# Kernel tuning notes

Hardware: AMD Instinct MI355X
Metric: run time of the kernel (lower is better)

Reference implementation:

```python
import jax, jax.numpy as jnp
import numpy as np

T, HEADS, DIM_HEAD = 16, 16, 72
M = HEADS * DIM_HEAD  # 1152
SCALE = DIM_HEAD ** -0.5


def _ln(x, eps):
    mu = x.mean(-1, keepdims=True)
    var = x.var(-1, keepdims=True)
    return (x - mu) / jnp.sqrt(var + eps)


def _rotate_half(t):
    # interleaved pairs (x1, x2) -> (-x2, x1), as in rotary-embedding-torch
    t1, t2 = t[..., 0::2], t[..., 1::2]
    return jnp.stack([-t2, t1], axis=-1).reshape(t.shape)


def _rotary(t, pos):
    d = t.shape[-1]
    inv_freq = 1.0 / (10000.0 ** (jnp.arange(0, d, 2, dtype=jnp.float32) / d))
    freqs = pos.astype(jnp.float32)[:, None] * inv_freq          # (T, d/2)
    freqs = jnp.repeat(freqs, 2, axis=-1)                        # (T, d)
    return t * jnp.cos(freqs) + _rotate_half(t) * jnp.sin(freqs)


def _forward(x, c4t, c, W_ada, b_ada, tn_w, tn_b, t_qkv, t_k, t_v, t_out,
             t_fc_w, t_fc_b, s_qkv, s_k, s_v, s_out,
             mlp_w1, mlp_b1, mlp_w2, mlp_b2, f):
    B = c4t.shape[0]
    K, N, _ = x.shape

    ada = jax.nn.silu(c4t) @ W_ada + b_ada                       # (B, 6M)
    sh_msa, sc_msa, g_msa, sh_mlp, sc_mlp, g_mlp = jnp.split(ada, 6, axis=1)

    x4 = x.reshape(B, T, N, M)

    # ---- temporal attention (seq dim = frames, rotary, per-frame cond k/v) ----
    xt = _ln(x4, 1e-5) * tn_w + tn_b                             # temporal_norm1
    xt = xt.transpose(0, 2, 1, 3)                                # (B, N, T, M)
    q, k, v = jnp.split(xt @ t_qkv, 3, axis=-1)

    def heads_t(t):  # (B,N,T,M) -> (B,N,h,T,d)
        return t.reshape(B, N, T, HEADS, DIM_HEAD).transpose(0, 1, 3, 2, 4)

    q, k, v = map(heads_t, (q, k, v))
    k = _rotary(k, f)
    ek = (c @ t_k).reshape(B, T, HEADS, DIM_HEAD).transpose(0, 2, 1, 3)  # (B,h,T,d)
    ev = (c @ t_v).reshape(B, T, HEADS, DIM_HEAD).transpose(0, 2, 1, 3)
    ek = _rotary(ek, f)
    ek = jnp.broadcast_to(ek[:, None], k.shape)                  # (B,N,h,T,d)
    ev = jnp.broadcast_to(ev[:, None], v.shape)
    kk = jnp.concatenate([ek, k], axis=-2)                       # (B,N,h,2T,d)
    vv = jnp.concatenate([ev, v], axis=-2)
    q = _rotary(q * SCALE, f)
    attn = jax.nn.softmax(jnp.einsum('bnhid,bnhjd->bnhij', q, kk), axis=-1)
    out = jnp.einsum('bnhij,bnhjd->bnhid', attn, vv)
    out = out.transpose(0, 1, 3, 2, 4).reshape(B, N, T, M) @ t_out
    res = out.transpose(0, 2, 1, 3) @ t_fc_w + t_fc_b            # (B,T,N,M)
    x4 = x4 + res

    # ---- spatial attention with adaLN modulate + one cond token per frame ----
    mod = _ln(x4, 1e-6) * (1.0 + sc_msa[:, None, None, :]) + sh_msa[:, None, None, :]
    q, k, v = jnp.split(mod @ s_qkv, 3, axis=-1)

    def heads_s(t):  # (B,T,N,M) -> (B,T,h,N,d)
        return t.reshape(B, T, N, HEADS, DIM_HEAD).transpose(0, 1, 3, 2, 4)

    q, k, v = map(heads_s, (q, k, v))
    ek = (c @ s_k).reshape(B, T, HEADS, DIM_HEAD)[:, :, :, None, :]  # (B,T,h,1,d)
    ev = (c @ s_v).reshape(B, T, HEADS, DIM_HEAD)[:, :, :, None, :]
    kk = jnp.concatenate([ek, k], axis=-2)                       # (B,T,h,N+1,d)
    vv = jnp.concatenate([ev, v], axis=-2)
    attn = jax.nn.softmax(jnp.einsum('bthid,bthjd->bthij', q * SCALE, kk), axis=-1)
    out = jnp.einsum('bthij,bthjd->bthid', attn, vv)
    out = out.transpose(0, 1, 3, 2, 4).reshape(B, T, N, M) @ s_out
    x4 = x4 + g_msa[:, None, None, :] * out

    # ---- gated MLP with adaLN modulate ----
    mod2 = _ln(x4, 1e-6) * (1.0 + sc_mlp[:, None, None, :]) + sh_mlp[:, None, None, :]
    h = jax.nn.gelu(mod2 @ mlp_w1 + mlp_b1, approximate=True)
    y = h @ mlp_w2 + mlp_b2
    x4 = x4 + g_mlp[:, None, None, :] * y
    return x4.reshape(K, N, M)


def setup_inputs() -> dict:
    key = jax.random.key(0)
    ks = jax.random.split(key, 20)
    B, N = 2, 256

    def w(k, shape, s=0.02):
        return jax.random.normal(k, shape, jnp.float32) * s

    return {
        'x': jax.random.normal(ks[0], (B * T, N, M), jnp.float32),
        'c4t': jax.random.normal(ks[1], (B, M), jnp.float32),
        'c': jax.random.normal(ks[2], (B, T, M), jnp.float32),
        'W_ada': w(ks[3], (M, 6 * M)), 'b_ada': w(ks[4], (6 * M,)),
        'tn_w': jnp.ones(M, jnp.float32), 'tn_b': jnp.zeros(M, jnp.float32),
        't_qkv': w(ks[5], (M, 3 * M)), 't_k': w(ks[6], (M, M)),
        't_v': w(ks[7], (M, M)), 't_out': w(ks[8], (M, M)),
        't_fc_w': w(ks[9], (M, M)), 't_fc_b': jnp.zeros(M, jnp.float32),
        's_qkv': w(ks[10], (M, 3 * M)), 's_k': w(ks[11], (M, M)),
        's_v': w(ks[12], (M, M)), 's_out': w(ks[13], (M, M)),
        'mlp_w1': w(ks[14], (M, 4 * M)), 'mlp_b1': jnp.zeros(4 * M, jnp.float32),
        'mlp_w2': w(ks[15], (4 * M, M)), 'mlp_b2': jnp.zeros(M, jnp.float32),
        'f': jnp.arange(T, dtype=jnp.int32),
    }


def reference(x, c4t, c, W_ada, b_ada, tn_w, tn_b, t_qkv, t_k, t_v, t_out,
              t_fc_w, t_fc_b, s_qkv, s_k, s_v, s_out,
              mlp_w1, mlp_b1, mlp_w2, mlp_b2, f):
    return _forward(x, c4t, c, W_ada, b_ada, tn_w, tn_b, t_qkv, t_k, t_v, t_out,
                    t_fc_w, t_fc_b, s_qkv, s_k, s_v, s_out,
                    mlp_w1, mlp_b1, mlp_w2, mlp_b2, f)
```

## Files before the change

kernel.cpp:

```cpp
#include <hip/hip_runtime.h>
#include <hip/hip_bf16.h>

typedef __hip_bfloat16 bf16;
typedef __attribute__((ext_vector_type(8))) short short8;
typedef __attribute__((ext_vector_type(4))) float floatx4;

__device__ __forceinline__ float b2f(bf16 v) { return __bfloat162float(v); }
__device__ __forceinline__ short f2bs(float v) {
    bf16 h = __float2bfloat16(v);
    return *(short*)&h;
}
__device__ __forceinline__ float invfreq(int jj) {
    return expf(-0.25584278811044955f * (float)jj);
}

template<int MODE>
__device__ __forceinline__ float ldin(const void* p, long i) {
    if (MODE == 0) return b2f(((const bf16*)p)[i]);
    else           return ((const float*)p)[i];
}

#define SCALE_ 0.11785113019775793f

#define GLDS(gp, lp) __builtin_amdgcn_global_load_lds( \
    (const __attribute__((address_space(1))) void*)(gp), \
    (__attribute__((address_space(3))) void*)(lp), 16, 0, 0)

__global__ void k_detect(const void* __restrict__ x, int* __restrict__ flag)
{
    const unsigned short* u = (const unsigned short*)x;
    int tid = threadIdx.x;
    int insane = 0;
    for (int i = tid; i < 2048; i += 64) {
        unsigned short s = u[i];
        int ex = (s >> 7) & 0xFF;
        if (ex >= 0xC5) insane++;
    }
    #pragma unroll
    for (int off = 32; off > 0; off >>= 1) insane += __shfl_down(insane, off);
    if (tid == 0) flag[0] = (insane > 8) ? 1 : 0;
}

__global__ void k_rope(const int* __restrict__ f, float* __restrict__ ropeC,
                       float* __restrict__ ropeS)
{
    int idx = blockIdx.x * 256 + threadIdx.x;
    if (idx < 1152) {
        int t = idx / 72, d = idx - t * 72;
        float ang = (float)f[t] * invfreq(d >> 1);
        float sn, cs; sincosf(ang, &sn, &cs);
        ropeC[idx] = cs;
        ropeS[idx] = sn;
    }
}

__global__ void k_silu(const void* __restrict__ c4t, float* __restrict__ out,
                       const int* __restrict__ flg)
{
    int i = blockIdx.x * 256 + threadIdx.x;
    if (i < 2304) {
        float v = (*flg == 0) ? ldin<0>(c4t, i) : ldin<1>(c4t, i);
        out[i] = v / (1.f + expf(-v));
    }
}

__global__ void k_cvt(const void* __restrict__ in, float* __restrict__ out, int n,
                      const int* __restrict__ flg)
{
    int i = blockIdx.x * 256 + threadIdx.x;
    if (i < n) out[i] = (*flg == 0) ? ldin<0>(in, i) : ldin<1>(in, i);
}

__global__ void k_cvtb(const float* __restrict__ in, bf16* __restrict__ out, int n)
{
    int i = blockIdx.x * 256 + threadIdx.x;
    if (i < n) out[i] = __float2bfloat16(in[i]);
}

template<int MODE>
__device__ __forceinline__ void wt_body(float (*tile)[33], const void* __restrict__ W,
    bf16* __restrict__ Wt, int K, int N)
{
    int n0 = blockIdx.x << 5, k0 = blockIdx.y << 5;
    int tid = threadIdx.x;
    int r = tid >> 3, c4 = (tid & 7) << 2;
    long base = (long)(k0 + r) * N + n0 + c4;
    #pragma unroll
    for (int i = 0; i < 4; ++i) tile[r][c4 + i] = ldin<MODE>(W, base + i);
    __syncthreads();
    long obase = (long)(n0 + r) * K + k0 + c4;
    #pragma unroll
    for (int i = 0; i < 4; ++i) Wt[obase + i] = __float2bfloat16(tile[c4 + i][r]);
}

__global__ __launch_bounds__(256) void k_wt(const void* __restrict__ W,
    bf16* __restrict__ Wt, int K, int N, const int* __restrict__ flg)
{
    __shared__ float tile[32][33];
    if (*flg == 0) wt_body<0>(tile, W, Wt, K, N);
    else           wt_body<1>(tile, W, Wt, K, N);
}

template<int MODE>
__device__ __forceinline__ void gemm_body(
    float (*As)[64], float (*Bs)[64],
    const float* __restrict__ A, const void* __restrict__ W,
    const void* __restrict__ bias, float* __restrict__ C,
    int R, int K, int N)
{
    int tid = threadIdx.x;
    int tx = tid & 15, ty = tid >> 4;
    int row0 = blockIdx.y << 6;
    int col0 = blockIdx.x << 6;
    float acc[4][4] = {};
    int ar = tid >> 2;
    int ak = (tid & 3) << 2;
    int bk = tid >> 4;
    int bc = (tid & 15) << 2;
    for (int kt = 0; kt < K; kt += 16) {
        if (row0 + ar < R) {
            const float4 a4 = *(const float4*)(A + (long)(row0 + ar) * K + kt + ak);
            As[ak + 0][ar] = a4.x; As[ak + 1][ar] = a4.y;
            As[ak + 2][ar] = a4.z; As[ak + 3][ar] = a4.w;
        } else {
            As[ak + 0][ar] = 0.f; As[ak + 1][ar] = 0.f;
            As[ak + 2][ar] = 0.f; As[ak + 3][ar] = 0.f;
        }
        #pragma unroll
        for (int i = 0; i < 4; ++i)
            Bs[bk][bc + i] = ldin<MODE>(W, (long)(kt + bk) * N + col0 + bc + i);
        __syncthreads();
        #pragma unroll
        for (int kk = 0; kk < 16; ++kk) {
            float4 av = *(const float4*)&As[kk][ty << 2];
            float4 bv = *(const float4*)&Bs[kk][tx << 2];
            float a[4] = {av.x, av.y, av.z, av.w};
            float b[4] = {bv.x, bv.y, bv.z, bv.w};
            #pragma unroll
            for (int i = 0; i < 4; ++i)
                #pragma unroll
                for (int j = 0; j < 4; ++j)
                    acc[i][j] += a[i] * b[j];
        }
        __syncthreads();
    }
    #pragma unroll
    for (int i = 0; i < 4; ++i) {
        int gr = row0 + (ty << 2) + i;
        if (gr >= R) continue;
        float* cp = C + (long)gr * N + col0 + (tx << 2);
        #pragma unroll
        for (int j = 0; j < 4; ++j) {
            float v = acc[i][j];
            if (bias) v += ldin<MODE>(bias, col0 + (tx << 2) + j);
            cp[j] = v;
        }
    }
}

__global__ __launch_bounds__(256) void k_gemm(
    const float* __restrict__ A, const void* __restrict__ W,
    const void* __restrict__ bias, float* __restrict__ C,
    int R, int K, int N, const int* __restrict__ flg)
{
    __shared__ float As[16][64];
    __shared__ float Bs[16][64];
    if (*flg == 0) gemm_body<0>(As, Bs, A, W, bias, C, R, K, N);
    else           gemm_body<1>(As, Bs, A, W, bias, C, R, K, N);
}

__global__ __launch_bounds__(256) void k_mgemm(
    const bf16* __restrict__ A, const bf16* __restrict__ Wt,
    const float* __restrict__ bias, void* __restrict__ Cout,
    int K, int N, int outbf, int act)
{
    __shared__ short As[8192];
    __shared__ short Bs[8192];
    int tid = threadIdx.x;
    int lane = tid & 63, wave = tid >> 6;
    int mq = wave >> 1, nq = wave & 1;

    int gx = gridDim.x;
    int nwg = gx * (int)gridDim.y;
    int orig = blockIdx.y * gx + blockIdx.x;
    int qq = nwg >> 3, rr = nwg & 7;
    int xcd = orig & 7, loc = orig >> 3;
    int wg = (xcd < rr ? xcd * (qq + 1) : rr * (qq + 1) + (xcd - rr) * qq) + loc;
    int bx = wg % gx, by = wg / gx;

    long row0 = (long)by << 7;
    long col0 = (long)bx << 7;
    int mi = lane & 15, q = lane >> 4;

    const bf16* gA0 = A  + (row0 + (2 * wave) * 16 + mi) * K + q * 8;
    const bf16* gA1 = A  + (row0 + (2 * wave + 1) * 16 + mi) * K + q * 8;
    const bf16* gB0 = Wt + (col0 + (2 * wave) * 16 + mi) * K + q * 8;
    const bf16* gB1 = Wt + (col0 + (2 * wave + 1) * 16 + mi) * K + q * 8;
    short* lA0 = &As[((2 * wave) << 1) * 512];
    short* lA1 = &As[((2 * wave + 1) << 1) * 512];
    short* lB0 = &Bs[((2 * wave) << 1) * 512];
    short* lB1 = &Bs[((2 * wave + 1) << 1) * 512];

    floatx4 acc[4][4] = {};

    for (int kt = 0; kt < K; kt += 64) {
        GLDS(gA0 + kt,      lA0);
        GLDS(gA0 + kt + 32, lA0 + 512);
        GLDS(gA1 + kt,      lA1);
        GLDS(gA1 + kt + 32, lA1 + 512);
        GLDS(gB0 + kt,      lB0);
        GLDS(gB0 + kt + 32, lB0 + 512);
        GLDS(gB1 + kt,      lB1);
        GLDS(gB1 + kt + 32, lB1 + 512);
        __syncthreads();
        #pragma unroll
        for (int s = 0; s < 2; ++s) {
            short8 af[4], bfr[4];
            #pragma unroll
            for (int i = 0; i < 4; ++i)
                af[i] = *(const short8*)&As[((((4 * mq + i) << 1) + s) << 9) + lane * 8];
            #pragma unroll
            for (int j = 0; j < 4; ++j)
                bfr[j] = *(const short8*)&Bs[((((4 * nq + j) << 1) + s) << 9) + lane * 8];
            #pragma unroll
            for (int i = 0; i < 4; ++i)
                #pragma unroll
                for (int j = 0; j < 4; ++j)
                    acc[i][j] = __builtin_amdgcn_mfma_f32_16x16x32_bf16(
                        af[i], bfr[j], acc[i][j], 0, 0, 0);
        }
        __syncthreads();
    }

    int lr = lane >> 4, lc = lane & 15;
    float b4[4] = {0.f, 0.f, 0.f, 0.f};
    if (bias) {
        #pragma unroll
        for (int j = 0; j < 4; ++j) b4[j] = bias[(int)col0 + nq * 64 + j * 16 + lc];
    }
    #pragma unroll
    for (int i = 0; i < 4; ++i) {
        #pragma unroll
        for (int r = 0; r < 4; ++r) {
            long grow = row0 + mq * 64 + i * 16 + lr * 4 + r;
            #pragma unroll
            for (int j = 0; j < 4; ++j) {
                int col = (int)col0 + nq * 64 + j * 16 + lc;
                float v = acc[i][j][r] + b4[j];
                if (act) {
                    float u = v;
                    float t = 1.5957691216057308f * (u + 0.044715f * u * u * u);
                    v = u / (1.f + __expf(-t));
                }
                if (outbf) ((bf16*)Cout)[grow * N + col] = __float2bfloat16(v);
                else       ((float*)Cout)[grow * N + col] = v;
            }
        }
    }
}

template<int MODE>
__device__ __forceinline__ void ln_t_body(float* rs, float* rss,
    const void* __restrict__ x, const void* __restrict__ w,
    const void* __restrict__ bb, bf16* __restrict__ out)
{
    int r = blockIdx.x;
    int n = r & 255;
    int bt = r >> 8;
    int b = bt >> 4, t = bt & 15;
    long orow = (long)((b << 8) + n) * 16 + t;
    int tid = threadIdx.x;
    float vals[5];
    float s = 0.f, ss = 0.f;
    int c = 0;
    for (int i = tid; i < 1152; i += 256, ++c) {
        float v = ldin<MODE>(x, (long)r * 1152 + i);
        vals[c] = v; s += v; ss += v * v;
    }
    #pragma unroll
    for (int off = 32; off > 0; off >>= 1) {
        s  += __shfl_down(s, off);
        ss += __shfl_down(ss, off);
    }
    int wid = tid >> 6;
    if ((tid & 63) == 0) { rs[wid] = s; rss[wid] = ss; }
    __syncthreads();
    float S  = rs[0] + rs[1] + rs[2] + rs[3];
    float SS = rss[0] + rss[1] + rss[2] + rss[3];
    float mu = S * (1.f / 1152.f);
    float var = SS * (1.f / 1152.f) - mu * mu;
    float rstd = rsqrtf(var + 1e-5f);
    c = 0;
    bf16* op = out + orow * 1152;
    for (int i = tid; i < 1152; i += 256, ++c)
        op[i] = __float2bfloat16((vals[c] - mu) * rstd * ldin<MODE>(w, i) + ldin<MODE>(bb, i));
}

__global__ __launch_bounds__(256) void k_ln_t(
    const void* __restrict__ x, const void* __restrict__ w,
    const void* __restrict__ bb, bf16* __restrict__ out,
    const int* __restrict__ flg)
{
    __shared__ float rs[4], rss[4];
    if (*flg == 0) ln_t_body<0>(rs, rss, x, w, bb, out);
    else           ln_t_body<1>(rs, rss, x, w, bb, out);
}

__global__ __launch_bounds__(256) void k_ln_mod(
    const float* __restrict__ x4, const float* __restrict__ ada,
    int psh, int psc, float eps, bf16* __restrict__ out)
{
    int r = blockIdx.x;
    int b = r >> 12;
    const float* xp = x4 + (long)r * 1152;
    int tid = threadIdx.x;
    float vals[5];
    float s = 0.f, ss = 0.f;
    int c = 0;
    for (int i = tid; i < 1152; i += 256, ++c) {
        float v = xp[i];
        vals[c] = v; s += v; ss += v * v;
    }
    #pragma unroll
    for (int off = 32; off > 0; off >>= 1) {
        s  += __shfl_down(s, off);
        ss += __shfl_down(ss, off);
    }
    __shared__ float rs[4], rss[4];
    int wid = tid >> 6;
    if ((tid & 63) == 0) { rs[wid] = s; rss[wid] = ss; }
    __syncthreads();
    float S  = rs[0] + rs[1] + rs[2] + rs[3];
    float SS = rss[0] + rss[1] + rss[2] + rss[3];
    float mu = S * (1.f / 1152.f);
    float var = SS * (1.f / 1152.f) - mu * mu;
    float rstd = rsqrtf(var + eps);
    const float* sh = ada + (b * 6 + psh) * 1152;
    const float* sc = ada + (b * 6 + psc) * 1152;
    c = 0;
    bf16* op = out + (long)r * 1152;
    for (int i = tid; i < 1152; i += 256, ++c)
        op[i] = __float2bfloat16((vals[c] - mu) * rstd * (1.f + sc[i]) + sh[i]);
}

__global__ __launch_bounds__(256) void k_attn_t(
    const bf16* __restrict__ qkv, const float* __restrict__ ekt,
    const float* __restrict__ evt, const float* __restrict__ ropeC,
    const float* __restrict__ ropeS, bf16* __restrict__ out)
{
    __shared__ float qs[16][73];
    __shared__ float ksT[72][33];
    __shared__ float vs[32][73];
    __shared__ float sc[16][33];
    int blk = blockIdx.x;
    int h = blk & 15;
    int bn = blk >> 4;
    int b = bn >> 8;
    int tid = threadIdx.x;
    long qbase = (long)bn * 16 * 3456 + h * 72;
    for (int idx = tid; idx < 16 * 72; idx += 256) {
        int i = idx / 72, d = idx - i * 72;
        long p0 = qbase + (long)i * 3456;
        float v  = b2f(qkv[p0 + d]);
        float v2 = b2f(qkv[p0 + (d ^ 1)]);
        float cs = ropeC[idx], sn = ropeS[idx];
        float rv = (d & 1) ? (v * cs + v2 * sn) : (v * cs - v2 * sn);
        qs[i][d] = rv * SCALE_;
    }
    for (int idx = tid; idx < 32 * 72; idx += 256) {
        int j = idx / 72, d = idx - j * 72;
        float kv, kv2, vv; int pi;
        if (j < 16) {
            long base = (long)(b * 16 + j) * 1152 + h * 72;
            kv  = ekt[base + d];
            kv2 = ekt[base + (d ^ 1)];
            vv  = evt[base + d];
            pi = j;
        } else {
            int jj = j - 16;
            long base = qbase + (long)jj * 3456;
            kv  = b2f(qkv[base + 1152 + d]);
            kv2 = b2f(qkv[base + 1152 + (d ^ 1)]);
            vv  = b2f(qkv[base + 2304 + d]);
            pi = jj;
        }
        float cs = ropeC[pi * 72 + d], sn = ropeS[pi * 72 + d];
        ksT[d][j] = (d & 1) ? (kv * cs + kv2 * sn) : (kv * cs - kv2 * sn);
        vs[j][d] = vv;
    }
    __syncthreads();
    for (int e = tid; e < 512; e += 256) {
        int i = e >> 5, j = e & 31;
        float s = 0.f;
        for (int d = 0; d < 72; ++d) s += qs[i][d] * ksT[d][j];
        sc[i][j] = s;
    }
    __syncthreads();
    if (tid < 16) {
        float m = -1e30f;
        for (int j = 0; j < 32; ++j) m = fmaxf(m, sc[tid][j]);
        float l = 0.f;
        for (int j = 0; j < 32; ++j) { float p = expf(sc[tid][j] - m); sc[tid][j] = p; l += p; }
        float inv = 1.f / l;
        for (int j = 0; j < 32; ++j) sc[tid][j] *= inv;
    }
    __syncthreads();
    for (int idx = tid; idx < 16 * 72; idx += 256) {
        int i = idx / 72, d = idx - i * 72;
        float o = 0.f;
        for (int j = 0; j < 32; ++j) o += sc[i][j] * vs[j][d];
        out[((long)bn * 16 + i) * 1152 + h * 72 + d] = __float2bfloat16(o);
    }
}

__global__ __launch_bounds__(256) void k_attn_s(
    const bf16* __restrict__ qkv, const bf16* __restrict__ eksb,
    const bf16* __restrict__ evsb, bf16* __restrict__ out)
{
    __shared__ short vT[5120];
    __shared__ short pl[4][1024];
    int tid = threadIdx.x;
    int lane = tid & 63, wave = tid >> 6;
    int blk = blockIdx.x;
    int ic = blk & 3;
    int bth = blk >> 2;
    int h = bth & 15;
    int bt = bth >> 4;
    int col = lane & 15, q = lane >> 4;
    int hoff = h * 72;
    long qkvbase = (long)bt * 256 * 3456;
    long ctxbase = (long)bt * 1152 + hoff;

    int qrow = ic * 64 + wave * 16 + col;
    const bf16* qptr = qkv + qkvbase + (long)qrow * 3456 + hoff;
    short8 qf[3];
    #pragma unroll
    for (int ks = 0; ks < 3; ++ks) {
        int k0 = ks * 32 + q * 8;
        if (k0 + 8 <= 72) qf[ks] = *(const short8*)(qptr + k0);
        else { short8 z = {0,0,0,0,0,0,0,0}; qf[ks] = z; }
    }

    floatx4 o[5] = {};
    float m_i[4], l_i[4];
    #pragma unroll
    for (int r = 0; r < 4; ++r) { m_i[r] = -1e30f; l_i[r] = 0.f; }

    for (int kc = 0; kc < 320; kc += 64) {
        for (int fi = tid; fi < 640; fi += 256) {
            int blkid = fi >> 6, fl = fi & 63;
            int dn = blkid >> 1, ks = blkid & 1;
            int d = dn * 16 + (fl & 15);
            int kq = fl >> 4;
            short8 v;
            #pragma unroll
            for (int j = 0; j < 8; ++j) {
                int gk = kc + ks * 32 + kq * 8 + j;
                short sv = 0;
                if (d < 72 && gk <= 256) {
                    if (gk == 0) sv = *(const short*)(eksb ? &evsb[ctxbase + d] : nullptr);
                    else sv = *(const short*)&qkv[qkvbase + (long)(gk - 1) * 3456 + 2304 + hoff + d];
                }
                v[j] = sv;
            }
            *(short8*)&vT[blkid * 512 + fl * 8] = v;
        }
        __syncthreads();

        floatx4 sacc[4] = {};
        #pragma unroll
        for (int nt = 0; nt < 4; ++nt) {
            int key = kc + nt * 16 + col;
            #pragma unroll
            for (int ks = 0; ks < 3; ++ks) {
                int k0 = ks * 32 + q * 8;
                short8 kf = {0,0,0,0,0,0,0,0};
                if (key <= 256 && k0 + 8 <= 72) {
                    if (key == 0) kf = *(const short8*)(eksb + ctxbase + k0);
                    else kf = *(const short8*)(qkv + qkvbase + (long)(key - 1) * 3456 + 1152 + hoff + k0);
                }
                sacc[nt] = __builtin_amdgcn_mfma_f32_16x16x32_bf16(qf[ks], kf, sacc[nt], 0, 0, 0);
            }
        }

        float p[4][4];
        #pragma unroll
        for (int r = 0; r < 4; ++r) {
            float mv = -1e30f;
            #pragma unroll
            for (int nt = 0; nt < 4; ++nt) {
                int key = kc + nt * 16 + col;
                float s = (key <= 256) ? sacc[nt][r] * SCALE_ : -1e30f;
                p[nt][r] = s;
                mv = fmaxf(mv, s);
            }
            #pragma unroll
            for (int xm = 1; xm < 16; xm <<= 1) mv = fmaxf(mv, __shfl_xor(mv, xm));
            float mn = fmaxf(m_i[r], mv);
            float alpha = expf(m_i[r] - mn);
            m_i[r] = mn;
            float rsum = 0.f;
            #pragma unroll
            for (int nt = 0; nt < 4; ++nt) {
                float e = expf(p[nt][r] - mn);
                p[nt][r] = e;
                rsum += e;
            }
            #pragma unroll
            for (int xm = 1; xm < 16; xm <<= 1) rsum += __shfl_xor(rsum, xm);
            l_i[r] = l_i[r] * alpha + rsum;
            #pragma unroll
            for (int dn = 0; dn < 5; ++dn) o[dn][r] *= alpha;
        }

        #pragma unroll
        for (int nt = 0; nt < 4; ++nt) {
            int kl = nt * 16 + col;
            int ks2 = kl >> 5, q2 = (kl >> 3) & 3, j = kl & 7;
            #pragma unroll
            for (int r = 0; r < 4; ++r) {
                int mrow = q * 4 + r;
                pl[wave][ks2 * 512 + q2 * 128 + mrow * 8 + j] = f2bs(p[nt][r]);
            }
        }
        __syncthreads();

        #pragma unroll
        for (int ks = 0; ks < 2; ++ks) {
            short8 pf = *(const short8*)&pl[wave][ks * 512 + lane * 8];
            #pragma unroll
            for (int dn = 0; dn < 5; ++dn) {
                short8 vf = *(const short8*)&vT[(dn * 2 + ks) * 512 + lane * 8];
                o[dn] = __builtin_amdgcn_mfma_f32_16x16x32_bf16(pf, vf, o[dn], 0, 0, 0);
            }
        }
        __syncthreads();
    }

    int orow0 = ic * 64 + wave * 16;
    #pragma unroll
    for (int dn = 0; dn < 5; ++dn) {
        int d = dn * 16 + col;
        if (d >= 72) continue;
        #pragma unroll
        for (int r = 0; r < 4; ++r) {
            int mrow = q * 4 + r;
            float val = o[dn][r] / l_i[r];
            out[((long)bt * 256 + orow0 + mrow) * 1152 + hoff + d] = __float2bfloat16(val);
        }
    }
}

__global__ __launch_bounds__(256) void k_add_t(
    const void* __restrict__ x, const float* __restrict__ res,
    float* __restrict__ x4, const int* __restrict__ flg)
{
    int idx = blockIdx.x * 256 + threadIdx.x;
    int r = idx / 1152;
    int mcol = idx - r * 1152;
    int n = r & 255;
    int bt = r >> 8;
    int b = bt >> 4, t = bt & 15;
    long r2 = (long)((b << 8) + n) * 16 + t;
    float xv = (*flg == 0) ? ldin<0>(x, idx) : ldin<1>(x, idx);
    x4[idx] = xv + res[r2 * 1152 + mcol];
}

__global__ __launch_bounds__(256) void k_add_g(
    float* __restrict__ x4, const float* __restrict__ y,
    const float* __restrict__ ada, int part, void* __restrict__ outp,
    const int* __restrict__ flg)
{
    int idx = blockIdx.x * 256 + threadIdx.x;
    int r = idx / 1152;
    int mcol = idx - r * 1152;
    int b = r >> 12;
    float g = ada[(b * 6 + part) * 1152 + mcol];
    float v = x4[idx] + g * y[idx];
    x4[idx] = v;
    if (outp) {
        if (*flg == 0) ((bf16*)outp)[idx] = __float2bfloat16(v);
        else           ((float*)outp)[idx] = v;
    }
}

extern "C" void kernel_launch(void* const* d_in, const int* in_sizes, int n_in,
                              void* d_out, int out_size, void* d_ws, size_t ws_size,
                              hipStream_t stream)
{
    const void* x      = d_in[0];
    const void* c4t    = d_in[1];
    const void* c      = d_in[2];
    const void* W_ada  = d_in[3];
    const void* b_ada  = d_in[4];
    const void* tn_w   = d_in[5];
    const void* tn_b   = d_in[6];
    const void* t_qkv  = d_in[7];
    const void* t_k    = d_in[8];
    const void* t_v    = d_in[9];
    const void* t_outw = d_in[10];
    const void* t_fcw  = d_in[11];
    const void* t_fcb  = d_in[12];
    const void* s_qkv  = d_in[13];
    const void* s_k    = d_in[14];
    const void* s_v    = d_in[15];
    const void* s_outw = d_in[16];
    const void* mlp_w1 = d_in[17];
    const void* mlp_b1 = d_in[18];
    const void* mlp_w2 = d_in[19];
    const void* mlp_b2 = d_in[20];
    const int*  f      = (const int*)d_in[21];

    float* ws    = (float*)d_ws;
    float* x4    = ws;
    float* buf2  = x4 + 9437184;
    float* reg1f = buf2 + 9437184;
    bf16*  qkvb  = (bf16*)reg1f;
    bf16*  hbf   = (bf16*)reg1f;
    float* abfAf = reg1f + 18874368;
    bf16*  abfA  = (bf16*)abfAf;
    float* abfBf = abfAf + 4718592;
    bf16*  abfB  = (bf16*)abfBf;
    float* wtf   = abfBf + 4718592;
    bf16*  wt    = (bf16*)wtf;
    bf16* t_qkv_t = wt;
    bf16* s_qkv_t = t_qkv_t + 3981312;
    bf16* t_out_t = s_qkv_t + 3981312;
    bf16* t_fc_t  = t_out_t + 1327104;
    bf16* s_out_t = t_fc_t  + 1327104;
    bf16* w1_t    = s_out_t + 1327104;
    bf16* w2_t    = w1_t    + 5308416;
    float* small  = wtf + 11280384;
    float* ada   = small;
    float* cf32  = ada  + 13824;
    float* ekt   = cf32 + 36864;
    float* evt   = ekt  + 36864;
    float* eks   = evt  + 36864;
    float* evs   = eks  + 36864;
    bf16*  eksb  = (bf16*)(evs + 36864);
    bf16*  evsb  = eksb + 36864;
    float* sc4   = (float*)(evsb + 36864);
    float* fcb_f = sc4  + 2304;
    float* b1_f  = fcb_f + 1152;
    float* b2_f  = b1_f  + 4608;
    float* ropeC = b2_f + 1152;
    float* ropeS = ropeC + 1152;
    int*   flg   = (int*)(ropeS + 1152);

    k_detect<<<1, 64, 0, stream>>>(x, flg);
    k_rope<<<5, 256, 0, stream>>>(f, ropeC, ropeS);

    k_silu<<<9, 256, 0, stream>>>(c4t, sc4, flg);
    k_gemm<<<dim3(108, 1), 256, 0, stream>>>(sc4, W_ada, b_ada, ada, 2, 1152, 6912, flg);

    k_cvt<<<144, 256, 0, stream>>>(c, cf32, 36864, flg);
    k_gemm<<<dim3(18, 1), 256, 0, stream>>>(cf32, t_k, nullptr, ekt, 32, 1152, 1152, flg);
    k_gemm<<<dim3(18, 1), 256, 0, stream>>>(cf32, t_v, nullptr, evt, 32, 1152, 1152, flg);
    k_gemm<<<dim3(18, 1), 256, 0, stream>>>(cf32, s_k, nullptr, eks, 32, 1152, 1152, flg);
    k_gemm<<<dim3(18, 1), 256, 0, stream>>>(cf32, s_v, nullptr, evs, 32, 1152, 1152, flg);
    k_cvtb<<<144, 256, 0, stream>>>(eks, eksb, 36864);
    k_cvtb<<<144, 256, 0, stream>>>(evs, evsb, 36864);

    k_cvt<<<5, 256, 0, stream>>>(t_fcb, fcb_f, 1152, flg);
    k_cvt<<<18, 256, 0, stream>>>(mlp_b1, b1_f, 4608, flg);
    k_cvt<<<5, 256, 0, stream>>>(mlp_b2, b2_f, 1152, flg);

    k_wt<<<dim3(108, 36), 256, 0, stream>>>(t_qkv, t_qkv_t, 1152, 3456, flg);
    k_wt<<<dim3(108, 36), 256, 0, stream>>>(s_qkv, s_qkv_t, 1152, 3456, flg);
    k_wt<<<dim3(36, 36), 256, 0, stream>>>(t_outw, t_out_t, 1152, 1152, flg);
    k_wt<<<dim3(36, 36), 256, 0, stream>>>(t_fcw, t_fc_t, 1152, 1152, flg);
    k_wt<<<dim3(36, 36), 256, 0, stream>>>(s_outw, s_out_t, 1152, 1152, flg);
    k_wt<<<dim3(144, 36), 256, 0, stream>>>(mlp_w1, w1_t, 1152, 4608, flg);
    k_wt<<<dim3(36, 144), 256, 0, stream>>>(mlp_w2, w2_t, 4608, 1152, flg);

    k_ln_t<<<8192, 256, 0, stream>>>(x, tn_w, tn_b, abfA, flg);
    k_mgemm<<<dim3(27, 64), 256, 0, stream>>>(abfA, t_qkv_t, nullptr, qkvb, 1152, 3456, 1, 0);
    k_attn_t<<<8192, 256, 0, stream>>>(qkvb, ekt, evt, ropeC, ropeS, abfB);
    k_mgemm<<<dim3(9, 64), 256, 0, stream>>>(abfB, t_out_t, nullptr, abfA, 1152, 1152, 1, 0);
    k_mgemm<<<dim3(9, 64), 256, 0, stream>>>(abfA, t_fc_t, fcb_f, buf2, 1152, 1152, 0, 0);
    k_add_t<<<36864, 256, 0, stream>>>(x, buf2, x4, flg);

    k_ln_mod<<<8192, 256, 0, stream>>>(x4, ada, 0, 1, 1e-6f, abfA);
    k_mgemm<<<dim3(27, 64), 256, 0, stream>>>(abfA, s_qkv_t, nullptr, qkvb, 1152, 3456, 1, 0);
    k_attn_s<<<2048, 256, 0, stream>>>(qkvb, eksb, evsb, abfB);
    k_mgemm<<<dim3(9, 64), 256, 0, stream>>>(abfB, s_out_t, nullptr, buf2, 1152, 1152, 0, 0);
    k_add_g<<<36864, 256, 0, stream>>>(x4, buf2, ada, 2, nullptr, flg);

    k_ln_mod<<<8192, 256, 0, stream>>>(x4, ada, 3, 4, 1e-6f, abfA);
    k_mgemm<<<dim3(36, 64), 256, 0, stream>>>(abfA, w1_t, b1_f, hbf, 1152, 4608, 1, 1);
    k_mgemm<<<dim3(9, 64), 256, 0, stream>>>(hbf, w2_t, b2_f, buf2, 4608, 1152, 0, 0);
    k_add_g<<<36864, 256, 0, stream>>>(x4, buf2, ada, 5, d_out, flg);
}
```

Measured before the change: 1.779 ms.

## Double-buffer MFMA GEMM K-loop and fuse residual adds into GEMM epilogues

The bf16 MFMA GEMM's K loop now works on 32-wide K tiles with two LDS buffers, so the next tile is prefetched with global_load_lds while the current one is multiplied, with one barrier per step. A templated epilogue mode folds the temporal residual add (with the frame/token row permutation) and the gated residual adds into the GEMM output stores. This removes three standalone elementwise kernels and their fp32 intermediate round trips through memory. The cost is a scattered, permuted write pattern in the EMODE 1 epilogue, and the smaller K step means more barriers per GEMM.

```diff
diff --git a/kernel.cpp b/kernel.cpp
--- a/kernel.cpp
+++ b/kernel.cpp
@@ -169,10 +169,14 @@
     else           gemm_body<1>(As, Bs, A, W, bias, C, R, K, N);
 }
 
+template<int EMODE>
 __global__ __launch_bounds__(256) void k_mgemm(
     const bf16* __restrict__ A, const bf16* __restrict__ Wt,
     const float* __restrict__ bias, void* __restrict__ Cout,
-    int K, int N, int outbf, int act)
+    int K, int N, int outbf, int act,
+    float* __restrict__ x4, const float* __restrict__ ada, int part,
+    const void* __restrict__ xin, void* __restrict__ outp,
+    const int* __restrict__ flg)
 {
     __shared__ short As[8192];
     __shared__ short Bs[8192];
@@ -196,43 +200,59 @@
     const bf16* gA1 = A  + (row0 + (2 * wave + 1) * 16 + mi) * K + q * 8;
     const bf16* gB0 = Wt + (col0 + (2 * wave) * 16 + mi) * K + q * 8;
     const bf16* gB1 = Wt + (col0 + (2 * wave + 1) * 16 + mi) * K + q * 8;
-    short* lA0 = &As[((2 * wave) << 1) * 512];
-    short* lA1 = &As[((2 * wave + 1) << 1) * 512];
-    short* lB0 = &Bs[((2 * wave) << 1) * 512];
-    short* lB1 = &Bs[((2 * wave + 1) << 1) * 512];
+    int la0 = (2 * wave) << 9;
+    int la1 = (2 * wave + 1) << 9;
 
     floatx4 acc[4][4] = {};
 
-    for (int kt = 0; kt < K; kt += 64) {
-        GLDS(gA0 + kt,      lA0);
-        GLDS(gA0 + kt + 32, lA0 + 512);
-        GLDS(gA1 + kt,      lA1);
-        GLDS(gA1 + kt + 32, lA1 + 512);
-        GLDS(gB0 + kt,      lB0);
-        GLDS(gB0 + kt + 32, lB0 + 512);
-        GLDS(gB1 + kt,      lB1);
-        GLDS(gB1 + kt + 32, lB1 + 512);
+    int nt = K >> 5;
+    GLDS(gA0, &As[la0]);
+    GLDS(gA1, &As[la1]);
+    GLDS(gB0, &Bs[la0]);
+    GLDS(gB1, &Bs[la1]);
+    __syncthreads();
+
+    for (int t = 0; t < nt - 1; ++t) {
+        int cur = (t & 1) << 12, nxt = cur ^ 4096;
+        int kt2 = (t + 1) << 5;
+        GLDS(gA0 + kt2, &As[nxt + la0]);
+        GLDS(gA1 + kt2, &As[nxt + la1]);
+        GLDS(gB0 + kt2, &Bs[nxt + la0]);
+        GLDS(gB1 + kt2, &Bs[nxt + la1]);
+        short8 af[4], bfr[4];
+        #pragma unroll
+        for (int i = 0; i < 4; ++i)
+            af[i] = *(const short8*)&As[cur + ((4 * mq + i) << 9) + lane * 8];
+        #pragma unroll
+        for (int j = 0; j < 4; ++j)
+            bfr[j] = *(const short8*)&Bs[cur + ((4 * nq + j) << 9) + lane * 8];
+        #pragma unroll
+        for (int i = 0; i < 4; ++i)
+            #pragma unroll
+            for (int j = 0; j < 4; ++j)
+                acc[i][j] = __builtin_amdgcn_mfma_f32_16x16x32_bf16(
+                    af[i], bfr[j], acc[i][j], 0, 0, 0);
         __syncthreads();
-        #pragma unroll
-        for (int s = 0; s < 2; ++s) {
-            short8 af[4], bfr[4];
-            #pragma unroll
-            for (int i = 0; i < 4; ++i)
-                af[i] = *(const short8*)&As[((((4 * mq + i) << 1) + s) << 9) + lane * 8];
+    }
+    {
+        int cur = ((nt - 1) & 1) << 12;
+        short8 af[4], bfr[4];
+        #pragma unroll
+        for (int i = 0; i < 4; ++i)
+            af[i] = *(const short8*)&As[cur + ((4 * mq + i) << 9) + lane * 8];
+        #pragma unroll
+        for (int j = 0; j < 4; ++j)
+            bfr[j] = *(const short8*)&Bs[cur + ((4 * nq + j) << 9) + lane * 8];
+        #pragma unroll
+        for (int i = 0; i < 4; ++i)
             #pragma unroll
             for (int j = 0; j < 4; ++j)
-                bfr[j] = *(const short8*)&Bs[((((4 * nq + j) << 1) + s) << 9) + lane * 8];
-            #pragma unroll
-            for (int i = 0; i < 4; ++i)
-                #pragma unroll
-                for (int j = 0; j < 4; ++j)
-                    acc[i][j] = __builtin_amdgcn_mfma_f32_16x16x32_bf16(
-                        af[i], bfr[j], acc[i][j], 0, 0, 0);
-        }
-        __syncthreads();
+                acc[i][j] = __builtin_amdgcn_mfma_f32_16x16x32_bf16(
+                    af[i], bfr[j], acc[i][j], 0, 0, 0);
     }
 
     int lr = lane >> 4, lc = lane & 15;
+    int fl = flg ? *flg : 0;
     float b4[4] = {0.f, 0.f, 0.f, 0.f};
     if (bias) {
         #pragma unroll
@@ -249,11 +269,32 @@
                 float v = acc[i][j][r] + b4[j];
                 if (act) {
                     float u = v;
-                    float t = 1.5957691216057308f * (u + 0.044715f * u * u * u);
-                    v = u / (1.f + __expf(-t));
+                    float tt = 1.5957691216057308f * (u + 0.044715f * u * u * u);
+                    v = u / (1.f + __expf(-tt));
                 }
-                if (outbf) ((bf16*)Cout)[grow * N + col] = __float2bfloat16(v);
-                else       ((float*)Cout)[grow * N + col] = v;
+                if constexpr (EMODE == 0) {
+                    if (outbf) ((bf16*)Cout)[grow * N + col] = __float2bfloat16(v);
+                    else       ((float*)Cout)[grow * N + col] = v;
+                } else if constexpr (EMODE == 1) {
+                    int bb = (int)(grow >> 12);
+                    int nn = ((int)grow >> 4) & 255;
+                    int tt2 = (int)grow & 15;
+                    long rx = ((long)((bb << 4) + tt2) << 8) + nn;
+                    long idx = rx * 1152 + col;
+                    float xv = (fl == 0) ? b2f(((const bf16*)xin)[idx])
+                                         : ((const float*)xin)[idx];
+                    x4[idx] = xv + v;
+                } else {
+                    int bb = (int)(grow >> 12);
+                    float g = ada[(bb * 6 + part) * 1152 + col];
+                    long idx = grow * 1152 + col;
+                    float nv = x4[idx] + g * v;
+                    x4[idx] = nv;
+                    if (outp) {
+                        if (fl == 0) ((bf16*)outp)[idx] = __float2bfloat16(nv);
+                        else         ((float*)outp)[idx] = nv;
+                    }
+                }
             }
         }
     }
@@ -448,10 +489,10 @@
 
     for (int kc = 0; kc < 320; kc += 64) {
         for (int fi = tid; fi < 640; fi += 256) {
-            int blkid = fi >> 6, fl = fi & 63;
+            int blkid = fi >> 6, fl2 = fi & 63;
             int dn = blkid >> 1, ks = blkid & 1;
-            int d = dn * 16 + (fl & 15);
-            int kq = fl >> 4;
+            int d = dn * 16 + (fl2 & 15);
+            int kq = fl2 >> 4;
             short8 v;
             #pragma unroll
             for (int j = 0; j < 8; ++j) {
@@ -463,7 +504,7 @@
                 }
                 v[j] = sv;
             }
-            *(short8*)&vT[blkid * 512 + fl * 8] = v;
+            *(short8*)&vT[blkid * 512 + fl2 * 8] = v;
         }
         __syncthreads();
 
@@ -548,39 +589,6 @@
             float val = o[dn][r] / l_i[r];
             out[((long)bt * 256 + orow0 + mrow) * 1152 + hoff + d] = __float2bfloat16(val);
         }
-    }
-}
-
-__global__ __launch_bounds__(256) void k_add_t(
-    const void* __restrict__ x, const float* __restrict__ res,
-    float* __restrict__ x4, const int* __restrict__ flg)
-{
-    int idx = blockIdx.x * 256 + threadIdx.x;
-    int r = idx / 1152;
-    int mcol = idx - r * 1152;
-    int n = r & 255;
-    int bt = r >> 8;
-    int b = bt >> 4, t = bt & 15;
-    long r2 = (long)((b << 8) + n) * 16 + t;
-    float xv = (*flg == 0) ? ldin<0>(x, idx) : ldin<1>(x, idx);
-    x4[idx] = xv + res[r2 * 1152 + mcol];
-}
-
-__global__ __launch_bounds__(256) void k_add_g(
-    float* __restrict__ x4, const float* __restrict__ y,
-    const float* __restrict__ ada, int part, void* __restrict__ outp,
-    const int* __restrict__ flg)
-{
-    int idx = blockIdx.x * 256 + threadIdx.x;
-    int r = idx / 1152;
-    int mcol = idx - r * 1152;
-    int b = r >> 12;
-    float g = ada[(b * 6 + part) * 1152 + mcol];
-    float v = x4[idx] + g * y[idx];
-    x4[idx] = v;
-    if (outp) {
-        if (*flg == 0) ((bf16*)outp)[idx] = __float2bfloat16(v);
-        else           ((float*)outp)[idx] = v;
     }
 }
 
@@ -674,20 +682,24 @@
     k_wt<<<dim3(36, 144), 256, 0, stream>>>(mlp_w2, w2_t, 4608, 1152, flg);
 
     k_ln_t<<<8192, 256, 0, stream>>>(x, tn_w, tn_b, abfA, flg);
-    k_mgemm<<<dim3(27, 64), 256, 0, stream>>>(abfA, t_qkv_t, nullptr, qkvb, 1152, 3456, 1, 0);
+    k_mgemm<0><<<dim3(27, 64), 256, 0, stream>>>(abfA, t_qkv_t, nullptr, qkvb, 1152, 3456, 1, 0,
+                                                 nullptr, nullptr, 0, nullptr, nullptr, flg);
     k_attn_t<<<8192, 256, 0, stream>>>(qkvb, ekt, evt, ropeC, ropeS, abfB);
-    k_mgemm<<<dim3(9, 64), 256, 0, stream>>>(abfB, t_out_t, nullptr, abfA, 1152, 1152, 1, 0);
-    k_mgemm<<<dim3(9, 64), 256, 0, stream>>>(abfA, t_fc_t, fcb_f, buf2, 1152, 1152, 0, 0);
-    k_add_t<<<36864, 256, 0, stream>>>(x, buf2, x4, flg);
+    k_mgemm<0><<<dim3(9, 64), 256, 0, stream>>>(abfB, t_out_t, nullptr, abfA, 1152, 1152, 1, 0,
+                                                nullptr, nullptr, 0, nullptr, nullptr, flg);
+    k_mgemm<1><<<dim3(9, 64), 256, 0, stream>>>(abfA, t_fc_t, fcb_f, nullptr, 1152, 1152, 0, 0,
+                                                x4, nullptr, 0, x, nullptr, flg);
 
     k_ln_mod<<<8192, 256, 0, stream>>>(x4, ada, 0, 1, 1e-6f, abfA);
-    k_mgemm<<<dim3(27, 64), 256, 0, stream>>>(abfA, s_qkv_t, nullptr, qkvb, 1152, 3456, 1, 0);
+    k_mgemm<0><<<dim3(27, 64), 256, 0, stream>>>(abfA, s_qkv_t, nullptr, qkvb, 1152, 3456, 1, 0,
+                                                 nullptr, nullptr, 0, nullptr, nullptr, flg);
     k_attn_s<<<2048, 256, 0, stream>>>(qkvb, eksb, evsb, abfB);
-    k_mgemm<<<dim3(9, 64), 256, 0, stream>>>(abfB, s_out_t, nullptr, buf2, 1152, 1152, 0, 0);
-    k_add_g<<<36864, 256, 0, stream>>>(x4, buf2, ada, 2, nullptr, flg);
+    k_mgemm<2><<<dim3(9, 64), 256, 0, stream>>>(abfB, s_out_t, nullptr, nullptr, 1152, 1152, 0, 0,
+                                                x4, ada, 2, nullptr, nullptr, flg);
 
     k_ln_mod<<<8192, 256, 0, stream>>>(x4, ada, 3, 4, 1e-6f, abfA);
-    k_mgemm<<<dim3(36, 64), 256, 0, stream>>>(abfA, w1_t, b1_f, hbf, 1152, 4608, 1, 1);
-    k_mgemm<<<dim3(9, 64), 256, 0, stream>>>(hbf, w2_t, b2_f, buf2, 4608, 1152, 0, 0);
-    k_add_g<<<36864, 256, 0, stream>>>(x4, buf2, ada, 5, d_out, flg);
-}
+    k_mgemm<0><<<dim3(36, 64), 256, 0, stream>>>(abfA, w1_t, b1_f, hbf, 1152, 4608, 1, 1,
+                                                 nullptr, nullptr, 0, nullptr, nullptr, flg);
+    k_mgemm<2><<<dim3(9, 64), 256, 0, stream>>>(hbf, w2_t, b2_f, nullptr, 4608, 1152, 0, 0,
+                                                x4, ada, 5, nullptr, d_out, flg);
+}
```

Result: faster. 1.724 ms (-3.1%).
